# Kernel optimization log

Hardware: AMD Instinct MI355X
Metric: run time of the kernel (lower is better)

## Reference

```python
import jax, jax.numpy as jnp
import numpy as np

DIM_Q = 1024
DIM_KV = 768
N_HEADS = 4


def setup_inputs() -> dict:
    key = jax.random.key(0)
    ks = jax.random.split(key, 7)
    b, lq, lkv = 4, 2048, 2048
    q = jax.random.normal(ks[0], (b, lq, DIM_Q), dtype=jnp.float32)
    kv = jax.random.normal(ks[1], (b, lkv, DIM_KV), dtype=jnp.float32)
    s_q = 1.0 / np.sqrt(DIM_Q)
    s_kv = 1.0 / np.sqrt(DIM_KV)
    Wq = jax.random.normal(ks[2], (DIM_Q, DIM_Q), dtype=jnp.float32) * s_q
    Wk = jax.random.normal(ks[3], (DIM_Q, DIM_KV), dtype=jnp.float32) * s_kv
    Wv = jax.random.normal(ks[4], (DIM_Q, DIM_KV), dtype=jnp.float32) * s_kv
    Wo = jax.random.normal(ks[5], (DIM_Q, DIM_Q), dtype=jnp.float32) * s_q
    bo = jax.random.normal(ks[6], (DIM_Q,), dtype=jnp.float32) * 0.01
    return {"q": q, "kv": kv, "Wq": Wq, "Wk": Wk, "Wv": Wv, "Wo": Wo, "bo": bo}


def _split_heads(x):
    # [b, l, d] -> [b, h, l, d/h]
    b, l, d = x.shape
    return x.reshape(b, l, N_HEADS, d // N_HEADS).transpose(0, 2, 1, 3)


def reference(q, kv, Wq, Wk, Wv, Wo, bo):
    qp = q @ Wq.T               # [b, lq, dim_q]
    kp = kv @ Wk.T              # [b, lkv, dim_q]
    vp = kv @ Wv.T              # [b, lkv, dim_q]
    qh, kh, vh = _split_heads(qp), _split_heads(kp), _split_heads(vp)
    scale = (DIM_Q // N_HEADS) ** (-0.5)
    scores = jnp.einsum('bhqd,bhkd->bhqk', qh, kh) * scale
    attn = jax.nn.softmax(scores, axis=-1)
    ctx = jnp.einsum('bhqk,bhkd->bhqd', attn, vh)  # [b, h, lq, hd]
    b, h, lq, hd = ctx.shape
    ctx = ctx.transpose(0, 2, 1, 3).reshape(b, lq, h * hd)
    return ctx @ Wo.T + bo
```

## Files before the change

kernel.cpp:

```cpp
#include <hip/hip_runtime.h>

#define DIMQ 1024
#define NH 4
#define HD 256
#define BSZ 4
#define LQ 2048
#define LKV 2048

typedef __attribute__((ext_vector_type(8))) short bf16x8;
typedef __attribute__((ext_vector_type(4))) float f32x4;

__device__ inline unsigned short f32_to_bf16(float f) {
  union { float f; unsigned u; } v; v.f = f;
  unsigned u = v.u;
  return (unsigned short)((u + 0x7fffu + ((u >> 16) & 1u)) >> 16);
}

__device__ inline uint4 ld8cvt(const float* p, float scale) {
  const float4 a = *(const float4*)p;
  const float4 b = *(const float4*)(p + 4);
  union { unsigned short s[8]; uint4 v; } r;
  r.s[0] = f32_to_bf16(a.x * scale); r.s[1] = f32_to_bf16(a.y * scale);
  r.s[2] = f32_to_bf16(a.z * scale); r.s[3] = f32_to_bf16(a.w * scale);
  r.s[4] = f32_to_bf16(b.x * scale); r.s[5] = f32_to_bf16(b.y * scale);
  r.s[6] = f32_to_bf16(b.z * scale); r.s[7] = f32_to_bf16(b.w * scale);
  return r.v;
}

__device__ __forceinline__ void gl2lds16(const void* gptr, void* lptr) {
  __builtin_amdgcn_global_load_lds(
      (const __attribute__((address_space(1))) void*)gptr,
      (__attribute__((address_space(3))) void*)lptr, 16, 0, 0);
}

__global__ __launch_bounds__(256)
void cvt5(const float* s0, const float* s1, const float* s2, const float* s3,
          const float* s4, unsigned short* d0, unsigned short* d1,
          unsigned short* d2, unsigned short* d3, unsigned short* d4,
          long n0, long n1, long n2, long n3, long n4,
          float c0, float c1, float c2, float c3, float c4) {
  const float* s; unsigned short* d; long n; float c;
  switch (blockIdx.y) {
    case 0: s = s0; d = d0; n = n0; c = c0; break;
    case 1: s = s1; d = d1; n = n1; c = c1; break;
    case 2: s = s2; d = d2; n = n2; c = c2; break;
    case 3: s = s3; d = d3; n = n3; c = c3; break;
    default: s = s4; d = d4; n = n4; c = c4; break;
  }
  long i = ((long)blockIdx.x * 256 + threadIdx.x) * 8;
  if (i < n) *(uint4*)(d + i) = ld8cvt(s + i, c);
}

__global__ __launch_bounds__(256)
void transpose_k(const unsigned short* __restrict__ vp,
                 unsigned short* __restrict__ vpT) {
  __shared__ unsigned short T[64][72];
  const int l0g = blockIdx.x * 64;
  const int b = l0g / LKV, l0 = l0g % LKV;
  const int n0 = blockIdx.y * 64;
  const int tid = threadIdx.x;
  const int r = tid >> 3, c = tid & 7;
#pragma unroll
  for (int p = 0; p < 2; ++p) {
    int row = p * 32 + r;
    *(uint4*)&T[row][c * 8] = *(const uint4*)(vp + (size_t)(l0g + row) * DIMQ + n0 + c * 8);
  }
  __syncthreads();
#pragma unroll
  for (int p = 0; p < 2; ++p) {
    int n = p * 32 + r;
    union { unsigned short s[8]; uint4 v; } t;
#pragma unroll
    for (int j = 0; j < 8; ++j) t.s[j] = T[c * 8 + j][n];
    *(uint4*)(vpT + ((size_t)b * DIMQ + n0 + n) * LKV + l0 + c * 8) = t.v;
  }
}

template<typename TOUT, bool HAS_BIAS>
__global__ __launch_bounds__(256)
void gemm_bt(const unsigned short* __restrict__ A,
             const unsigned short* __restrict__ Bm,
             const float* __restrict__ bias,
             TOUT* __restrict__ C,
             int M, int N, int K) {
  __shared__ alignas(16) unsigned short As[128 * 32];
  __shared__ alignas(16) unsigned short Bs[128 * 32];
  const int tid = threadIdx.x;
  const int lane = tid & 63;
  const int wave = tid >> 6;
  const int wr = (wave >> 1) * 64, wc = (wave & 1) * 64;
  const int l15 = lane & 15, quad = lane >> 4;
  const int lr = lane >> 2, lc = lane & 3;
  const int m0 = blockIdx.x * 128;
  const int n0 = blockIdx.y * 128;

  f32x4 acc[4][4] = {};
  const int nK = K >> 5;
  for (int kt = 0; kt < nK; ++kt) {
    const int k0 = kt << 5;
    __syncthreads();
#pragma unroll
    for (int i = 0; i < 2; ++i) {
      int c = wave * 2 + i;
      gl2lds16(A + (size_t)(m0 + c * 16 + lr) * K + k0 + lc * 8, As + c * 512);
      gl2lds16(Bm + (size_t)(n0 + c * 16 + lr) * K + k0 + lc * 8, Bs + c * 512);
    }
    __syncthreads();
    bf16x8 af[4], bfr[4];
#pragma unroll
    for (int i = 0; i < 4; ++i)
      af[i] = *(const bf16x8*)(As + (wr + i * 16 + l15) * 32 + quad * 8);
#pragma unroll
    for (int j = 0; j < 4; ++j)
      bfr[j] = *(const bf16x8*)(Bs + (wc + j * 16 + l15) * 32 + quad * 8);
#pragma unroll
    for (int i = 0; i < 4; ++i)
#pragma unroll
      for (int j = 0; j < 4; ++j)
        acc[i][j] = __builtin_amdgcn_mfma_f32_16x16x32_bf16(af[i], bfr[j], acc[i][j], 0, 0, 0);
  }

#pragma unroll
  for (int j = 0; j < 4; ++j) {
    int n = n0 + wc + j * 16 + l15;
    float bv = 0.f;
    if (HAS_BIAS) bv = bias[n];
#pragma unroll
    for (int i = 0; i < 4; ++i) {
      int mb = m0 + wr + i * 16 + quad * 4;
#pragma unroll
      for (int r = 0; r < 4; ++r) {
        float v = acc[i][j][r] + bv;
        if constexpr (sizeof(TOUT) == 2)
          C[(size_t)(mb + r) * N + n] = f32_to_bf16(v);
        else
          C[(size_t)(mb + r) * N + n] = v;
      }
    }
  }
}

__global__ __launch_bounds__(256, 2)
void attn(const unsigned short* __restrict__ qp,
          const unsigned short* __restrict__ kp,
          const unsigned short* __restrict__ vpT,
          unsigned short* __restrict__ ctx) {
  __shared__ alignas(16) unsigned short Ks[8 * 64 * 32];
  __shared__ alignas(16) unsigned short Vt[2 * 256 * 32];
  __shared__ alignas(16) unsigned short Ps[4][16 * 72];
  const int tid = threadIdx.x, lane = tid & 63, wave = tid >> 6;
  const int l15 = lane & 15, quad = lane >> 4;
  const int lr = lane >> 2, lc = lane & 3;
  const int b = blockIdx.z, h = blockIdx.y;
  const int q0 = blockIdx.x * 64;
  const size_t base = (size_t)b * LQ * DIMQ + h * HD;

  bf16x8 qf[8];
  const unsigned short* qrow = qp + base + (size_t)(q0 + wave * 16 + l15) * DIMQ;
#pragma unroll
  for (int s = 0; s < 8; ++s)
    qf[s] = *(const bf16x8*)(qrow + s * 32 + quad * 8);

  f32x4 oacc[16] = {};
  float lrow[4] = {0.f, 0.f, 0.f, 0.f};

  const unsigned short* kb = kp + base;
  const unsigned short* vtb = vpT + ((size_t)b * DIMQ + h * HD) * LKV;

  for (int kv0 = 0; kv0 < LKV; kv0 += 64) {
    __syncthreads();
#pragma unroll
    for (int i = 0; i < 8; ++i) {
      int c = i * 4 + wave, s = c & 7, g = c >> 3;
      gl2lds16(kb + (size_t)(kv0 + g * 16 + lr) * DIMQ + s * 32 + lc * 8,
               Ks + s * 2048 + g * 512);
    }
#pragma unroll
    for (int i = 0; i < 8; ++i) {
      int c = i * 4 + wave, u = c >> 4, g = c & 15;
      gl2lds16(vtb + (size_t)(g * 16 + lr) * LKV + kv0 + u * 32 + lc * 8,
               Vt + u * 8192 + g * 512);
    }
    __syncthreads();

    f32x4 sacc[4] = {};
#pragma unroll
    for (int s = 0; s < 8; ++s)
#pragma unroll
      for (int j = 0; j < 4; ++j) {
        bf16x8 kf = *(const bf16x8*)(Ks + s * 2048 + (j * 16 + l15) * 32 + quad * 8);
        sacc[j] = __builtin_amdgcn_mfma_f32_16x16x32_bf16(qf[s], kf, sacc[j], 0, 0, 0);
      }

#pragma unroll
    for (int i = 0; i < 4; ++i) {
      float ps = 0.f;
#pragma unroll
      for (int j = 0; j < 4; ++j) {
        float p = __expf(sacc[j][i]);
        ps += p;
        Ps[wave][(quad * 4 + i) * 72 + j * 16 + l15] = f32_to_bf16(p);
      }
      lrow[i] += ps;
    }

#pragma unroll
    for (int u = 0; u < 2; ++u) {
      bf16x8 pf = *(const bf16x8*)(Ps[wave] + l15 * 72 + u * 32 + quad * 8);
#pragma unroll
      for (int t = 0; t < 16; ++t) {
        bf16x8 vf = *(const bf16x8*)(Vt + u * 8192 + (t * 16 + l15) * 32 + quad * 8);
        oacc[t] = __builtin_amdgcn_mfma_f32_16x16x32_bf16(pf, vf, oacc[t], 0, 0, 0);
      }
    }
  }

  float inv[4];
#pragma unroll
  for (int r = 0; r < 4; ++r) {
    float l = lrow[r];
    l += __shfl_xor(l, 1);
    l += __shfl_xor(l, 2);
    l += __shfl_xor(l, 4);
    l += __shfl_xor(l, 8);
    inv[r] = 1.0f / l;
  }
  unsigned short* cb = ctx + base;
#pragma unroll
  for (int t = 0; t < 16; ++t) {
    int col = t * 16 + l15;
#pragma unroll
    for (int r = 0; r < 4; ++r) {
      int row = q0 + wave * 16 + quad * 4 + r;
      cb[(size_t)row * DIMQ + col] = f32_to_bf16(oacc[t][r] * inv[r]);
    }
  }
}

extern "C" void kernel_launch(void* const* d_in, const int* in_sizes, int n_in,
                              void* d_out, int out_size, void* d_ws, size_t ws_size,
                              hipStream_t stream) {
  const float* q  = (const float*)d_in[0];
  const float* kv = (const float*)d_in[1];
  const float* Wq = (const float*)d_in[2];
  const float* Wk = (const float*)d_in[3];
  const float* Wv = (const float*)d_in[4];
  const float* Wo = (const float*)d_in[5];
  const float* bo = (const float*)d_in[6];
  float* out = (float*)d_out;

  const long NQ = (long)BSZ * LQ * DIMQ;
  const long NKV = (long)BSZ * LKV * 768;
  const long NWQ = (long)DIMQ * DIMQ;
  const long NWK = (long)DIMQ * 768;

  unsigned short* qp = (unsigned short*)d_out;
  unsigned short* kp = qp + NQ;
  unsigned short* kv_bf = (unsigned short*)d_ws;
  unsigned short* Wq_bf = kv_bf + NKV;
  unsigned short* Wk_bf = Wq_bf + NWQ;
  unsigned short* Wv_bf = Wk_bf + NWK;
  unsigned short* Wo_bf = Wv_bf + NWK;
  unsigned short* BUF1  = Wo_bf + NWQ;
  unsigned short* vpT   = BUF1 + NQ;

  dim3 blk(256);
  const int M = BSZ * LQ;

  cvt5<<<dim3(3072, 5), blk, 0, stream>>>(kv, Wq, Wk, Wv, Wo,
                                          kv_bf, Wq_bf, Wk_bf, Wv_bf, Wo_bf,
                                          NKV, NWQ, NWK, NWK, NWQ,
                                          1.0f, 0.0625f, 1.0f, 1.0f, 1.0f);
  gemm_bt<unsigned short, false><<<dim3(M/128, DIMQ/128), blk, 0, stream>>>(kv_bf, Wk_bf, nullptr, kp,   M, DIMQ, 768);
  gemm_bt<unsigned short, false><<<dim3(M/128, DIMQ/128), blk, 0, stream>>>(kv_bf, Wv_bf, nullptr, BUF1, M, DIMQ, 768);
  transpose_k<<<dim3(M/64, DIMQ/64), blk, 0, stream>>>(BUF1, vpT);
  cvt5<<<dim3(4096, 1), blk, 0, stream>>>(q, nullptr, nullptr, nullptr, nullptr,
                                          BUF1, nullptr, nullptr, nullptr, nullptr,
                                          NQ, 0, 0, 0, 0,
                                          1.0f, 0.f, 0.f, 0.f, 0.f);
  gemm_bt<unsigned short, false><<<dim3(M/128, DIMQ/128), blk, 0, stream>>>(BUF1, Wq_bf, nullptr, qp, M, DIMQ, 1024);
  attn<<<dim3(LQ/64, NH, BSZ), blk, 0, stream>>>(qp, kp, vpT, BUF1);
  gemm_bt<float, true><<<dim3(M/128, DIMQ/128), blk, 0, stream>>>(BUF1, Wo_bf, bo, out, M, DIMQ, 1024);
}
```

Baseline: 333.6 us.

## Fuse K and V projections into one GEMM and deepen GEMM k-tile to 64

```diff
diff --git a/kernel.cpp b/kernel.cpp
--- a/kernel.cpp
+++ b/kernel.cpp
@@ -6,6 +6,7 @@
 #define BSZ 4
 #define LQ 2048
 #define LKV 2048
+#define KVN 2048
 
 typedef __attribute__((ext_vector_type(8))) short bf16x8;
 typedef __attribute__((ext_vector_type(4))) float f32x4;
@@ -53,7 +54,8 @@
 
 __global__ __launch_bounds__(256)
 void transpose_k(const unsigned short* __restrict__ vp,
-                 unsigned short* __restrict__ vpT) {
+                 unsigned short* __restrict__ vpT,
+                 int src_stride, int src_off) {
   __shared__ unsigned short T[64][72];
   const int l0g = blockIdx.x * 64;
   const int b = l0g / LKV, l0 = l0g % LKV;
@@ -63,7 +65,8 @@
 #pragma unroll
   for (int p = 0; p < 2; ++p) {
     int row = p * 32 + r;
-    *(uint4*)&T[row][c * 8] = *(const uint4*)(vp + (size_t)(l0g + row) * DIMQ + n0 + c * 8);
+    *(uint4*)&T[row][c * 8] =
+        *(const uint4*)(vp + (size_t)(l0g + row) * src_stride + src_off + n0 + c * 8);
   }
   __syncthreads();
 #pragma unroll
@@ -83,41 +86,42 @@
              const float* __restrict__ bias,
              TOUT* __restrict__ C,
              int M, int N, int K) {
-  __shared__ alignas(16) unsigned short As[128 * 32];
-  __shared__ alignas(16) unsigned short Bs[128 * 32];
+  __shared__ alignas(16) unsigned short As[128 * 64];
+  __shared__ alignas(16) unsigned short Bs[128 * 64];
   const int tid = threadIdx.x;
   const int lane = tid & 63;
   const int wave = tid >> 6;
   const int wr = (wave >> 1) * 64, wc = (wave & 1) * 64;
   const int l15 = lane & 15, quad = lane >> 4;
-  const int lr = lane >> 2, lc = lane & 3;
+  const int srow = lane >> 3, scol = lane & 7;
   const int m0 = blockIdx.x * 128;
   const int n0 = blockIdx.y * 128;
 
   f32x4 acc[4][4] = {};
-  const int nK = K >> 5;
-  for (int kt = 0; kt < nK; ++kt) {
-    const int k0 = kt << 5;
-    __syncthreads();
-#pragma unroll
-    for (int i = 0; i < 2; ++i) {
-      int c = wave * 2 + i;
-      gl2lds16(A + (size_t)(m0 + c * 16 + lr) * K + k0 + lc * 8, As + c * 512);
-      gl2lds16(Bm + (size_t)(n0 + c * 16 + lr) * K + k0 + lc * 8, Bs + c * 512);
-    }
-    __syncthreads();
-    bf16x8 af[4], bfr[4];
-#pragma unroll
-    for (int i = 0; i < 4; ++i)
-      af[i] = *(const bf16x8*)(As + (wr + i * 16 + l15) * 32 + quad * 8);
-#pragma unroll
-    for (int j = 0; j < 4; ++j)
-      bfr[j] = *(const bf16x8*)(Bs + (wc + j * 16 + l15) * 32 + quad * 8);
-#pragma unroll
-    for (int i = 0; i < 4; ++i)
+  for (int k0 = 0; k0 < K; k0 += 64) {
+    __syncthreads();
+#pragma unroll
+    for (int i = 0; i < 4; ++i) {
+      int c = wave * 4 + i;
+      gl2lds16(A + (size_t)(m0 + c * 8 + srow) * K + k0 + scol * 8, As + c * 512);
+      gl2lds16(Bm + (size_t)(n0 + c * 8 + srow) * K + k0 + scol * 8, Bs + c * 512);
+    }
+    __syncthreads();
+#pragma unroll
+    for (int kh = 0; kh < 2; ++kh) {
+      bf16x8 af[4], bfr[4];
+#pragma unroll
+      for (int i = 0; i < 4; ++i)
+        af[i] = *(const bf16x8*)(As + (wr + i * 16 + l15) * 64 + kh * 32 + quad * 8);
 #pragma unroll
       for (int j = 0; j < 4; ++j)
-        acc[i][j] = __builtin_amdgcn_mfma_f32_16x16x32_bf16(af[i], bfr[j], acc[i][j], 0, 0, 0);
+        bfr[j] = *(const bf16x8*)(Bs + (wc + j * 16 + l15) * 64 + kh * 32 + quad * 8);
+#pragma unroll
+      for (int i = 0; i < 4; ++i)
+#pragma unroll
+        for (int j = 0; j < 4; ++j)
+          acc[i][j] = __builtin_amdgcn_mfma_f32_16x16x32_bf16(af[i], bfr[j], acc[i][j], 0, 0, 0);
+    }
   }
 
 #pragma unroll
@@ -142,7 +146,7 @@
 
 __global__ __launch_bounds__(256, 2)
 void attn(const unsigned short* __restrict__ qp,
-          const unsigned short* __restrict__ kp,
+          const unsigned short* __restrict__ kpv,
           const unsigned short* __restrict__ vpT,
           unsigned short* __restrict__ ctx) {
   __shared__ alignas(16) unsigned short Ks[8 * 64 * 32];
@@ -164,7 +168,7 @@
   f32x4 oacc[16] = {};
   float lrow[4] = {0.f, 0.f, 0.f, 0.f};
 
-  const unsigned short* kb = kp + base;
+  const unsigned short* kb = kpv + (size_t)b * LKV * KVN + h * HD;
   const unsigned short* vtb = vpT + ((size_t)b * DIMQ + h * HD) * LKV;
 
   for (int kv0 = 0; kv0 < LKV; kv0 += 64) {
@@ -172,7 +176,7 @@
 #pragma unroll
     for (int i = 0; i < 8; ++i) {
       int c = i * 4 + wave, s = c & 7, g = c >> 3;
-      gl2lds16(kb + (size_t)(kv0 + g * 16 + lr) * DIMQ + s * 32 + lc * 8,
+      gl2lds16(kb + (size_t)(kv0 + g * 16 + lr) * KVN + s * 32 + lc * 8,
                Ks + s * 2048 + g * 512);
     }
 #pragma unroll
@@ -254,15 +258,16 @@
   const long NWQ = (long)DIMQ * DIMQ;
   const long NWK = (long)DIMQ * 768;
 
-  unsigned short* qp = (unsigned short*)d_out;
-  unsigned short* kp = qp + NQ;
+  unsigned short* q_bf = (unsigned short*)d_out;
+  unsigned short* kpv  = (unsigned short*)d_out;
   unsigned short* kv_bf = (unsigned short*)d_ws;
-  unsigned short* Wq_bf = kv_bf + NKV;
+  unsigned short* ctx   = kv_bf;
+  unsigned short* Wq_bf = kv_bf + NQ;
   unsigned short* Wk_bf = Wq_bf + NWQ;
   unsigned short* Wv_bf = Wk_bf + NWK;
   unsigned short* Wo_bf = Wv_bf + NWK;
-  unsigned short* BUF1  = Wo_bf + NWQ;
-  unsigned short* vpT   = BUF1 + NQ;
+  unsigned short* qp    = Wo_bf + NWQ;
+  unsigned short* vpT   = qp + NQ;
 
   dim3 blk(256);
   const int M = BSZ * LQ;
@@ -271,14 +276,13 @@
                                           kv_bf, Wq_bf, Wk_bf, Wv_bf, Wo_bf,
                                           NKV, NWQ, NWK, NWK, NWQ,
                                           1.0f, 0.0625f, 1.0f, 1.0f, 1.0f);
-  gemm_bt<unsigned short, false><<<dim3(M/128, DIMQ/128), blk, 0, stream>>>(kv_bf, Wk_bf, nullptr, kp,   M, DIMQ, 768);
-  gemm_bt<unsigned short, false><<<dim3(M/128, DIMQ/128), blk, 0, stream>>>(kv_bf, Wv_bf, nullptr, BUF1, M, DIMQ, 768);
-  transpose_k<<<dim3(M/64, DIMQ/64), blk, 0, stream>>>(BUF1, vpT);
   cvt5<<<dim3(4096, 1), blk, 0, stream>>>(q, nullptr, nullptr, nullptr, nullptr,
-                                          BUF1, nullptr, nullptr, nullptr, nullptr,
+                                          q_bf, nullptr, nullptr, nullptr, nullptr,
                                           NQ, 0, 0, 0, 0,
                                           1.0f, 0.f, 0.f, 0.f, 0.f);
-  gemm_bt<unsigned short, false><<<dim3(M/128, DIMQ/128), blk, 0, stream>>>(BUF1, Wq_bf, nullptr, qp, M, DIMQ, 1024);
-  attn<<<dim3(LQ/64, NH, BSZ), blk, 0, stream>>>(qp, kp, vpT, BUF1);
-  gemm_bt<float, true><<<dim3(M/128, DIMQ/128), blk, 0, stream>>>(BUF1, Wo_bf, bo, out, M, DIMQ, 1024);
-}
+  gemm_bt<unsigned short, false><<<dim3(M/128, DIMQ/128), blk, 0, stream>>>(q_bf, Wq_bf, nullptr, qp, M, DIMQ, 1024);
+  gemm_bt<unsigned short, false><<<dim3(M/128, KVN/128), blk, 0, stream>>>(kv_bf, Wk_bf, nullptr, kpv, M, KVN, 768);
+  transpose_k<<<dim3(M/64, DIMQ/64), blk, 0, stream>>>(kpv, vpT, KVN, 1024);
+  attn<<<dim3(LQ/64, NH, BSZ), blk, 0, stream>>>(qp, kpv, vpT, ctx);
+  gemm_bt<float, true><<<dim3(M/128, DIMQ/128), blk, 0, stream>>>(ctx, Wo_bf, bo, out, M, DIMQ, 1024);
+}
```

Result: no change. 327.3 us (-1.9%).
